# Kernel optimization log

Hardware: AMD Instinct MI355X
Metric: run time of the kernel (lower is better)

The kernel has to match this reference:

```python
import jax, jax.numpy as jnp
import numpy as np

N = 50000       # nodes
E = 400000      # edges (avg degree 8)
IN, HID, OUT, ED = 128, 256, 128, 64
EXP = 2          # GENConv MLP expansion
EPS_MSG = 1e-7   # GENConv eps added to relu(msg)
EPS_BN = 1e-5    # BatchNorm eps
EPS_SM = 1e-16   # PyG softmax denominator eps


def _lin(key, fi, fo):
    w = jax.random.normal(key, (fi, fo), jnp.float32) / np.float32(np.sqrt(fi))
    return w, jnp.zeros((fo,), jnp.float32)


def _layer_params(key, fi, fo, ed):
    ks = jax.random.split(key, 5)
    Wsrc, bsrc = _lin(ks[0], fi, fo)
    Wdst, bdst = _lin(ks[1], fi, fo)
    We, be = _lin(ks[2], ed, fo)
    W1, b1 = _lin(ks[3], fo, fo * EXP)
    W2, b2 = _lin(ks[4], fo * EXP, fo)
    g = jnp.ones((fo * EXP,), jnp.float32)   # BN gamma
    bt = jnp.zeros((fo * EXP,), jnp.float32) # BN beta
    return dict(Wsrc=Wsrc, bsrc=bsrc, Wdst=Wdst, bdst=bdst, We=We, be=be,
                W1=W1, b1=b1, g=g, bt=bt, W2=W2, b2=b2)


def setup_inputs() -> dict:
    key = jax.random.key(0)
    k0, k1, k2, k3, k4 = jax.random.split(key, 5)
    inp = {
        'x': jax.random.normal(k0, (N, IN), jnp.float32),
        'edge_index': jax.random.randint(k1, (2, E), 0, N, jnp.int32),
        'edge_attr': jax.random.normal(k2, (E, ED), jnp.float32),
    }
    for pref, p in (('l1_', _layer_params(k3, IN, HID, ED)),
                    ('l2_', _layer_params(k4, HID, OUT, ED))):
        for n, v in p.items():
            inp[pref + n] = v
    return inp


def _genconv(x, src, dst, ea, Wsrc, bsrc, Wdst, bdst, We, be, W1, b1, g, bt, W2, b2):
    n = x.shape[0]
    h = x @ Wsrc + bsrc                          # [N, F] lin_src
    e = ea @ We + be                             # [E, F] lin_edge
    msg = jax.nn.relu(h[src] + e) + EPS_MSG      # [E, F] message
    # softmax aggregation over destination nodes (t = 1.0)
    mx = jax.ops.segment_max(msg, dst, num_segments=n)
    ex = jnp.exp(msg - mx[dst])
    den = jax.ops.segment_sum(ex, dst, num_segments=n)
    alpha = ex / (den[dst] + EPS_SM)
    agg = jax.ops.segment_sum(alpha * msg, dst, num_segments=n)  # [N, F]
    out = agg + (x @ Wdst + bdst)                # residual lin_dst
    # MLP: Linear -> BatchNorm(train stats) -> ReLU -> Linear
    h1 = out @ W1 + b1                           # [N, 2F]
    mu = h1.mean(0)
    var = h1.var(0)
    h1 = (h1 - mu) * jax.lax.rsqrt(var + EPS_BN) * g + bt
    return jax.nn.relu(h1) @ W2 + b2


def reference(x, edge_index, edge_attr,
              l1_Wsrc, l1_bsrc, l1_Wdst, l1_bdst, l1_We, l1_be,
              l1_W1, l1_b1, l1_g, l1_bt, l1_W2, l1_b2,
              l2_Wsrc, l2_bsrc, l2_Wdst, l2_bdst, l2_We, l2_be,
              l2_W1, l2_b1, l2_g, l2_bt, l2_W2, l2_b2):
    src, dst = edge_index[0], edge_index[1]
    h = _genconv(x, src, dst, edge_attr,
                 l1_Wsrc, l1_bsrc, l1_Wdst, l1_bdst, l1_We, l1_be,
                 l1_W1, l1_b1, l1_g, l1_bt, l1_W2, l1_b2)
    h = jax.nn.relu(h)
    return _genconv(h, src, dst, edge_attr,
                    l2_Wsrc, l2_bsrc, l2_Wdst, l2_bdst, l2_We, l2_be,
                    l2_W1, l2_b1, l2_g, l2_bt, l2_W2, l2_b2)
```

## Files before the change

kernel.cpp:

```cpp
#include <hip/hip_runtime.h>

typedef unsigned short u16;
typedef unsigned int u32;
typedef __attribute__((ext_vector_type(8))) short sv8;
typedef __attribute__((ext_vector_type(4))) float fv4;
typedef __attribute__((ext_vector_type(4))) unsigned short us4;
typedef __attribute__((ext_vector_type(2))) unsigned short us2;

__device__ __forceinline__ u16 f2b(float x) {
    union { float f; u32 u; } a; a.f = x;
    u32 r = a.u + 0x7FFFu + ((a.u >> 16) & 1u);
    return (u16)(r >> 16);
}
__device__ __forceinline__ float b2f(u16 h) {
    union { u32 u; float f; } a; a.u = ((u32)h) << 16;
    return a.f;
}

__device__ __forceinline__ void gll16(const void* g, void* l) {
    __builtin_amdgcn_global_load_lds((__attribute__((address_space(1))) void*)g,
                                     (__attribute__((address_space(3))) void*)l,
                                     16, 0, 0);
}

template<bool AF32, bool AAFF, int EPI, bool STATS>
__global__ __launch_bounds__(256) void k_gemm(
    const void* __restrict__ Aptr, const u16* __restrict__ Wt,
    const float* __restrict__ bias, void* __restrict__ Cptr,
    int M, int K, int F,
    const float* __restrict__ sc, const float* __restrict__ sh,
    float* __restrict__ sums, float* __restrict__ sumsq)
{
    __shared__ u16 As[64][36];
    __shared__ u16 Bs[64][36];
    __shared__ u16 Cs[64][68];
    const int t = threadIdx.x, w = t >> 6, l = t & 63;
    const int n0 = blockIdx.x * 64, m0 = blockIdx.y * 64;
    const int arow = t >> 2, acol = (t & 3) << 3;
    const size_t gr = (size_t)(m0 + arow < M ? m0 + arow : M - 1);

    fv4 acc[4] = {};

    for (int k0 = 0; k0 < K; k0 += 32) {
        sv8 av;
        if constexpr (AF32) {
            const float* Af = (const float*)Aptr;
            fv4 u0 = *(const fv4*)(Af + gr * K + k0 + acol);
            fv4 u1 = *(const fv4*)(Af + gr * K + k0 + acol + 4);
            #pragma unroll
            for (int j = 0; j < 4; ++j) { av[j] = (short)f2b(u0[j]); av[j + 4] = (short)f2b(u1[j]); }
        } else if constexpr (AAFF) {
            sv8 v = *(const sv8*)((const u16*)Aptr + gr * K + k0 + acol);
            fv4 c0 = *(const fv4*)(sc + k0 + acol), c1 = *(const fv4*)(sc + k0 + acol + 4);
            fv4 d0 = *(const fv4*)(sh + k0 + acol), d1 = *(const fv4*)(sh + k0 + acol + 4);
            #pragma unroll
            for (int j = 0; j < 4; ++j) {
                av[j]     = (short)f2b(fmaxf(b2f((u16)v[j])     * c0[j] + d0[j], 0.f));
                av[j + 4] = (short)f2b(fmaxf(b2f((u16)v[j + 4]) * c1[j] + d1[j], 0.f));
            }
        } else {
            av = *(const sv8*)((const u16*)Aptr + gr * K + k0 + acol);
        }
        *(sv8*)&As[arow][acol] = av;
        *(sv8*)&Bs[arow][acol] = *(const sv8*)(Wt + (size_t)(n0 + arow) * K + k0 + acol);
        __syncthreads();

        sv8 a = *(const sv8*)&As[(w << 4) + (l & 15)][(l >> 4) << 3];
        #pragma unroll
        for (int ct = 0; ct < 4; ++ct) {
            sv8 b = *(const sv8*)&Bs[(ct << 4) + (l & 15)][(l >> 4) << 3];
            acc[ct] = __builtin_amdgcn_mfma_f32_16x16x32_bf16(a, b, acc[ct], 0, 0, 0);
        }
        __syncthreads();
    }

    const int lr0 = (w << 4) + ((l >> 4) << 2);
    #pragma unroll
    for (int ct = 0; ct < 4; ++ct) {
        const int col = (ct << 4) + (l & 15);
        const float bv = bias[n0 + col];
        float s = 0.f, s2 = 0.f;
        #pragma unroll
        for (int r = 0; r < 4; ++r) {
            const int lrow = lr0 + r;
            const bool valid = (m0 + lrow) < M;
            float v = acc[ct][r] + bv;
            if constexpr (STATS) { if (valid) { s += v; s2 += v * v; } }
            if constexpr (EPI == 1) v = fmaxf(v, 0.f);
            if constexpr (EPI == 3) {
                if (valid) ((float*)Cptr)[(size_t)(m0 + lrow) * F + n0 + col] = v;
            } else {
                Cs[lrow][col] = f2b(v);
            }
        }
        if constexpr (STATS) {
            s  += __shfl_xor(s, 16);  s  += __shfl_xor(s, 32);
            s2 += __shfl_xor(s2, 16); s2 += __shfl_xor(s2, 32);
            if (l < 16) { unsafeAtomicAdd(&sums[n0 + col], s); unsafeAtomicAdd(&sumsq[n0 + col], s2); }
        }
    }
    if constexpr (EPI != 3) {
        __syncthreads();
        const int lrow = t >> 2, c0 = (t & 3) << 4;
        if (m0 + lrow < M) {
            u16* Cb = (u16*)Cptr + (size_t)(m0 + lrow) * F + n0 + c0;
            *(sv8*)Cb       = *(const sv8*)&Cs[lrow][c0];
            *(sv8*)(Cb + 8) = *(const sv8*)&Cs[lrow][c0 + 8];
        }
    }
}

template<int FN>
__global__ __launch_bounds__(256) void k_egemm3(
    const float* __restrict__ ea, const int* __restrict__ perm,
    const u16* __restrict__ Wt, const float* __restrict__ bias,
    u16* __restrict__ Cbuf)
{
    __shared__ u16 Bs[FN * 64];
    const int t = threadIdx.x, w = t >> 6, l = t & 63;
    const int m0 = blockIdx.x * 64;

    constexpr int BISS = FN / 32;
    #pragma unroll
    for (int i = 0; i < BISS; ++i) {
        int slot = ((w * BISS + i) << 6) + l;
        int row = slot >> 3, g = (slot & 7) ^ (row & 7);
        gll16(Wt + (size_t)row * 64 + g * 8, Bs + ((w * BISS + i) << 6) * 8);
    }

    const int g0 = l >> 4;
    const int gr = m0 + (w << 4) + (l & 15);
    const int prow = perm[gr];
    const float* ar = ea + (size_t)prow * 64 + (g0 << 3);
    fv4 u0 = *(const fv4*)ar;
    fv4 u1 = *(const fv4*)(ar + 4);
    fv4 u2 = *(const fv4*)(ar + 32);
    fv4 u3 = *(const fv4*)(ar + 36);
    sv8 a0, a1;
    #pragma unroll
    for (int j = 0; j < 4; ++j) {
        a0[j] = (short)f2b(u0[j]); a0[j + 4] = (short)f2b(u1[j]);
        a1[j] = (short)f2b(u2[j]); a1[j + 4] = (short)f2b(u3[j]);
    }
    __syncthreads();

    fv4 acc[FN / 16];
    #pragma unroll
    for (int ct = 0; ct < FN / 16; ++ct) {
        int Brow = (ct << 4) + (l & 15);
        sv8 b0 = *(const sv8*)&Bs[(Brow * 8 + ((g0)     ^ (Brow & 7))) * 8];
        sv8 b1 = *(const sv8*)&Bs[(Brow * 8 + ((g0 + 4) ^ (Brow & 7))) * 8];
        fv4 z = {};
        z = __builtin_amdgcn_mfma_f32_16x16x32_bf16(a0, b0, z, 0, 0, 0);
        acc[ct] = __builtin_amdgcn_mfma_f32_16x16x32_bf16(a1, b1, z, 0, 0, 0);
    }

    const int r0 = (w << 4) + ((l >> 4) << 2);
    #pragma unroll
    for (int ct = 0; ct < FN / 16; ++ct) {
        const int col = (ct << 4) + (l & 15);
        const float bv = bias[col];
        #pragma unroll
        for (int r = 0; r < 4; ++r) {
            const int row = m0 + r0 + r;
            u32 my = (u32)f2b(acc[ct][r] + bv);
            u32 ot = (u32)__shfl_xor((int)my, 1);
            if (!(l & 1))
                *(u32*)(Cbuf + (size_t)row * FN + col) = (my & 0xFFFFu) | (ot << 16);
        }
    }
}

__global__ void k_hist(const int* __restrict__ dst, int* __restrict__ counts, int E) {
    int i = blockIdx.x * 256 + threadIdx.x;
    if (i < E) atomicAdd(&counts[dst[i]], 1);
}

__global__ __launch_bounds__(256) void k_psum(const int* __restrict__ counts,
                                              int* __restrict__ bsum, int n) {
    int i = blockIdx.x * 256 + threadIdx.x;
    int v = (i < n) ? counts[i] : 0;
    #pragma unroll
    for (int o = 1; o < 64; o <<= 1) v += __shfl_xor(v, o);
    __shared__ int ws[4];
    if ((threadIdx.x & 63) == 0) ws[threadIdx.x >> 6] = v;
    __syncthreads();
    if (threadIdx.x == 0) bsum[blockIdx.x] = ws[0] + ws[1] + ws[2] + ws[3];
}

__global__ __launch_bounds__(256) void k_bscan(const int* __restrict__ bsum,
                                               int* __restrict__ boff, int nb) {
    __shared__ int sm[256];
    int t = threadIdx.x;
    int v = (t < nb) ? bsum[t] : 0;
    sm[t] = v; __syncthreads();
    #pragma unroll
    for (int o = 1; o < 256; o <<= 1) {
        int u = (t >= o) ? sm[t - o] : 0;
        __syncthreads();
        sm[t] += u;
        __syncthreads();
    }
    if (t < nb) boff[t] = sm[t] - v;
}

__global__ __launch_bounds__(256) void k_windp(const int* __restrict__ counts,
                                               const int* __restrict__ boff,
                                               int* __restrict__ indptr,
                                               int* __restrict__ cursors, int n) {
    __shared__ int sm[256];
    const int t = threadIdx.x, i = blockIdx.x * 256 + t;
    int v = (i < n) ? counts[i] : 0;
    sm[t] = v; __syncthreads();
    #pragma unroll
    for (int o = 1; o < 256; o <<= 1) {
        int u = (t >= o) ? sm[t - o] : 0;
        __syncthreads();
        sm[t] += u;
        __syncthreads();
    }
    int excl = sm[t] - v + boff[blockIdx.x];
    if (i < n) { indptr[i] = excl; cursors[i] = excl; }
    if (i == n - 1) indptr[n] = excl + v;
}

__global__ void k_scatter(const int* __restrict__ dst, const int* __restrict__ src,
                          int* __restrict__ cursors, int* __restrict__ perm,
                          int* __restrict__ srcp, int E) {
    int i = blockIdx.x * 256 + threadIdx.x;
    if (i < E) {
        int p = atomicAdd(&cursors[dst[i]], 1);
        perm[p] = i;
        srcp[p] = src[i];
    }
}

template<int F, int VPT>
__global__ __launch_bounds__(256) void k_agg(
    const u16* __restrict__ e, const u16* __restrict__ hhd,
    const int* __restrict__ srcp, const int* __restrict__ indptr,
    u16* __restrict__ out, int N)
{
    const int nid = blockIdx.x * 4 + (threadIdx.x >> 6);
    if (nid >= N) return;
    const int c0 = (threadIdx.x & 63) * VPT;
    const int S = 2 * F;
    const int p0 = indptr[nid], p1 = indptr[nid + 1];
    float den[VPT] = {}, num[VPT] = {};
    for (int p = p0; p < p1; ++p) {
        const int s = srcp[p];
        u16 ev[VPT], hv[VPT];
        if constexpr (VPT == 4) {
            *(us4*)ev = *(const us4*)&e[(size_t)p * F + c0];
            *(us4*)hv = *(const us4*)&hhd[(size_t)s * S + c0];
        } else {
            *(us2*)ev = *(const us2*)&e[(size_t)p * F + c0];
            *(us2*)hv = *(const us2*)&hhd[(size_t)s * S + c0];
        }
        #pragma unroll
        for (int j = 0; j < VPT; ++j) {
            float x = fmaxf(b2f(ev[j]) + b2f(hv[j]), 0.f) + 1e-7f;
            float ex = __expf(x);
            den[j] += ex;
            num[j] += ex * x;
        }
    }
    #pragma unroll
    for (int j = 0; j < VPT; ++j) {
        float o = num[j] / (den[j] + 1e-16f) + b2f(hhd[(size_t)nid * S + F + c0 + j]);
        out[(size_t)nid * F + c0 + j] = f2b(o);
    }
}

struct WtDesc { const float* W; u16* D; int K; int F; int end; };
struct WtPack { WtDesc d[10]; };

__global__ void k_wtall(WtPack p, int total) {
    int i = blockIdx.x * 256 + threadIdx.x;
    if (i >= total) return;
    int s = 0, base = 0;
    while (i >= p.d[s].end) { base = p.d[s].end; ++s; }
    int loc = i - base;
    int K = p.d[s].K, F = p.d[s].F;
    int f = loc / K, k = loc - f * K;
    p.d[s].D[loc] = f2b(p.d[s].W[(size_t)k * F + f]);
}

__global__ void k_bcat(const float* __restrict__ bsrc1, const float* __restrict__ bdst1,
                       const float* __restrict__ bsrc2, const float* __restrict__ bdst2,
                       float* __restrict__ bcat1, float* __restrict__ bcat2) {
    int t = threadIdx.x;
    bcat1[t] = bsrc1[t];
    bcat1[256 + t] = bdst1[t];
    if (t < 128) {
        bcat2[t] = bsrc2[t];
        bcat2[128 + t] = bdst2[t];
    }
}

__global__ void k_bnfinal(const float* __restrict__ sums, const float* __restrict__ sumsq,
                          const float* __restrict__ g, const float* __restrict__ bt,
                          float* __restrict__ scale, float* __restrict__ shift,
                          int C, float invN)
{
    int c = blockIdx.x * 256 + threadIdx.x;
    if (c < C) {
        float mu  = sums[c] * invN;
        float var = sumsq[c] * invN - mu * mu;
        float s   = g[c] * rsqrtf(var + 1e-5f);
        scale[c] = s;
        shift[c] = bt[c] - mu * s;
    }
}

extern "C" void kernel_launch(void* const* d_in, const int* in_sizes, int n_in,
                              void* d_out, int out_size, void* d_ws, size_t ws_size,
                              hipStream_t stream)
{
    const int IN = 128, HID = 256, OUT = 128, ED = 64;
    const int N = in_sizes[0] / IN;
    const int E = in_sizes[1] / 2;

    const float* x   = (const float*)d_in[0];
    const int*   src = (const int*)d_in[1];
    const int*   dst = src + E;
    const float* ea  = (const float*)d_in[2];
    auto F32 = [&](int i) { return (const float*)d_in[i]; };
    const float *Wsrc1 = F32(3),  *bsrc1 = F32(4),  *Wdst1 = F32(5),  *bdst1 = F32(6),
                *We1   = F32(7),  *be1   = F32(8),  *W11   = F32(9),  *b11   = F32(10),
                *g1    = F32(11), *bt1   = F32(12), *W21   = F32(13), *b21   = F32(14);
    const float *Wsrc2 = F32(15), *bsrc2 = F32(16), *Wdst2 = F32(17), *bdst2 = F32(18),
                *We2   = F32(19), *be2   = F32(20), *W12   = F32(21), *b12   = F32(22),
                *g2    = F32(23), *bt2   = F32(24), *W22   = F32(25), *b22   = F32(26);

    char* wp = (char*)d_ws;
    auto carve = [&](size_t bytes) -> void* {
        void* r = (void*)wp; wp += (bytes + 255) & ~(size_t)255; return r;
    };
    u16* wcat1  = (u16*)carve((size_t)HID * IN * 2);
    u16* wdst1t = (u16*)carve((size_t)HID * IN * 2);
    u16* we1t   = (u16*)carve((size_t)HID * ED * 2);
    u16* w11t   = (u16*)carve((size_t)(2 * HID) * HID * 2);
    u16* w21t   = (u16*)carve((size_t)HID * (2 * HID) * 2);
    u16* wcat2  = (u16*)carve((size_t)OUT * HID * 2);
    u16* wdst2t = (u16*)carve((size_t)OUT * HID * 2);
    u16* we2t   = (u16*)carve((size_t)OUT * ED * 2);
    u16* w12t   = (u16*)carve((size_t)(2 * OUT) * OUT * 2);
    u16* w22t   = (u16*)carve((size_t)OUT * (2 * OUT) * 2);
    int* counts  = (int*)carve((size_t)N * 4);
    int* indptr  = (int*)carve((size_t)(N + 1) * 4);
    int* cursors = (int*)carve((size_t)N * 4);
    int* perm    = (int*)carve((size_t)E * 4);
    int* srcp    = (int*)carve((size_t)E * 4);
    int* bsum    = (int*)carve((size_t)256 * 4);
    int* boff    = (int*)carve((size_t)256 * 4);
    u16* hhd  = (u16*)carve((size_t)N * 512 * 2);
    u16* x2   = (u16*)carve((size_t)N * HID * 2);
    u16* ebuf = (u16*)carve((size_t)E * HID * 2);
    float* stats1 = (float*)carve((size_t)1024 * 4);
    float* stats2 = (float*)carve((size_t)512 * 4);
    float* ss1    = (float*)carve((size_t)1024 * 4);
    float* ss2    = (float*)carve((size_t)512 * 4);
    float* bcat1  = (float*)carve((size_t)512 * 4);
    float* bcat2  = (float*)carve((size_t)256 * 4);
    u16* h1 = ebuf;

    hipMemsetAsync(counts, 0, (size_t)N * 4, stream);
    hipMemsetAsync(stats1, 0, (size_t)(1024 + 512) * 4, stream);
    k_hist<<<dim3((E + 255) / 256), dim3(256), 0, stream>>>(dst, counts, E);
    const int nb = (N + 255) / 256;
    k_psum<<<dim3(nb), dim3(256), 0, stream>>>(counts, bsum, N);
    k_bscan<<<dim3(1), dim3(256), 0, stream>>>(bsum, boff, nb);
    k_windp<<<dim3(nb), dim3(256), 0, stream>>>(counts, boff, indptr, cursors, N);
    k_scatter<<<dim3((E + 255) / 256), dim3(256), 0, stream>>>(dst, src, cursors, perm, srcp, E);

    WtPack wpk; int acc_end = 0;
    auto addw = [&](int idx, const float* W, u16* D, int K, int F) {
        acc_end += K * F;
        wpk.d[idx] = WtDesc{W, D, K, F, acc_end};
    };
    addw(0, Wsrc1, wcat1,  IN, HID);   addw(1, Wdst1, wdst1t, IN, HID);
    addw(2, We1,   we1t,   ED, HID);   addw(3, W11,   w11t,   HID, 2 * HID);
    addw(4, W21,   w21t,   2 * HID, HID);
    addw(5, Wsrc2, wcat2,  HID, OUT);  addw(6, Wdst2, wdst2t, HID, OUT);
    addw(7, We2,   we2t,   ED, OUT);   addw(8, W12,   w12t,   OUT, 2 * OUT);
    addw(9, W22,   w22t,   2 * OUT, OUT);
    k_wtall<<<dim3((acc_end + 255) / 256), dim3(256), 0, stream>>>(wpk, acc_end);
    k_bcat<<<dim3(1), dim3(256), 0, stream>>>(bsrc1, bdst1, bsrc2, bdst2, bcat1, bcat2);

    const int gm = (N + 63) / 64;

    k_gemm<true, false, 0, false><<<dim3(8, gm), dim3(256), 0, stream>>>(
        x, wcat1, bcat1, hhd, N, IN, 512, nullptr, nullptr, nullptr, nullptr);
    k_egemm3<256><<<dim3(E / 64), dim3(256), 0, stream>>>(ea, perm, we1t, be1, ebuf);
    k_agg<256, 4><<<dim3((N + 3) / 4), dim3(256), 0, stream>>>(ebuf, hhd, srcp, indptr, x2, N);
    k_gemm<false, false, 0, true><<<dim3(8, gm), dim3(256), 0, stream>>>(
        x2, w11t, b11, h1, N, HID, 512, nullptr, nullptr, stats1, stats1 + 512);
    k_bnfinal<<<dim3(2), dim3(256), 0, stream>>>(
        stats1, stats1 + 512, g1, bt1, ss1, ss1 + 512, 512, 1.f / N);
    k_gemm<false, true, 1, false><<<dim3(4, gm), dim3(256), 0, stream>>>(
        h1, w21t, b21, x2, N, 512, HID, ss1, ss1 + 512, nullptr, nullptr);

    k_gemm<false, false, 0, false><<<dim3(4, gm), dim3(256), 0, stream>>>(
        x2, wcat2, bcat2, hhd, N, HID, 256, nullptr, nullptr, nullptr, nullptr);
    k_egemm3<128><<<dim3(E / 64), dim3(256), 0, stream>>>(ea, perm, we2t, be2, ebuf);
    k_agg<128, 2><<<dim3((N + 3) / 4), dim3(256), 0, stream>>>(ebuf, hhd, srcp, indptr, x2, N);
    k_gemm<false, false, 0, true><<<dim3(4, gm), dim3(256), 0, stream>>>(
        x2, w12t, b12, h1, N, OUT, 256, nullptr, nullptr, stats2, stats2 + 256);
    k_bnfinal<<<dim3(1), dim3(256), 0, stream>>>(
        stats2, stats2 + 256, g2, bt2, ss2, ss2 + 256, 256, 1.f / N);
    k_gemm<false, true, 3, false><<<dim3(2, gm), dim3(256), 0, stream>>>(
        h1, w22t, b22, d_out, N, HID, OUT, ss2, ss2 + 256, nullptr, nullptr);
}
```

Before: 699.9 us.

## Keep full weight panel resident in LDS with persistent row-tile GEMM loop

Replaces the K-tiled GEMM, which staged A and B through LDS with two barriers per k-step, by a kernel that loads a 64-column weight panel for the whole K into swizzled LDS once via global_load_lds. Each block then loops over many row tiles, streaming A straight from global memory into registers. MFMA operands are swapped so each lane holds four consecutive output columns, which allows vector stores without the LDS staging buffer. BatchNorm statistics are accumulated per block and reduced with fewer atomics. The cost is large LDS usage for K=512 (64 KB), which lowers occupancy, and a fixed grid size that may underfill or imbalance the GPU.

Result: slower. 833.7 us (+19.1%).

```diff
diff --git a/kernel.cpp b/kernel.cpp
--- a/kernel.cpp
+++ b/kernel.cpp
@@ -23,89 +23,112 @@
                                      16, 0, 0);
 }
 
-template<bool AF32, bool AAFF, int EPI, bool STATS>
-__global__ __launch_bounds__(256) void k_gemm(
+template<int K, int EPI, bool AF32, bool AAFF, bool STATS>
+__global__ __launch_bounds__(256) void k_ngemm(
     const void* __restrict__ Aptr, const u16* __restrict__ Wt,
     const float* __restrict__ bias, void* __restrict__ Cptr,
-    int M, int K, int F,
+    int M, int F,
     const float* __restrict__ sc, const float* __restrict__ sh,
     float* __restrict__ sums, float* __restrict__ sumsq)
 {
-    __shared__ u16 As[64][36];
-    __shared__ u16 Bs[64][36];
-    __shared__ u16 Cs[64][68];
+    constexpr int GPR = K / 8;
+    __shared__ u16 Ws[64 * K];
     const int t = threadIdx.x, w = t >> 6, l = t & 63;
-    const int n0 = blockIdx.x * 64, m0 = blockIdx.y * 64;
-    const int arow = t >> 2, acol = (t & 3) << 3;
-    const size_t gr = (size_t)(m0 + arow < M ? m0 + arow : M - 1);
-
-    fv4 acc[4] = {};
-
-    for (int k0 = 0; k0 < K; k0 += 32) {
-        sv8 av;
-        if constexpr (AF32) {
-            const float* Af = (const float*)Aptr;
-            fv4 u0 = *(const fv4*)(Af + gr * K + k0 + acol);
-            fv4 u1 = *(const fv4*)(Af + gr * K + k0 + acol + 4);
+    const int q = l >> 4;
+    const int n0 = blockIdx.x * 64;
+
+    #pragma unroll
+    for (int i = 0; i < K / 32; ++i) {
+        int slotbase = (w * (K / 32) + i) << 6;
+        int slot = slotbase + l;
+        int row = slot / GPR;
+        int g = slot & (GPR - 1);
+        int gs = (g & ~7) | ((g & 7) ^ (row & 7));
+        gll16(Wt + (size_t)(n0 + row) * K + gs * 8, Ws + slotbase * 8);
+    }
+    __syncthreads();
+
+    float sacc[16] = {}, s2acc[16] = {};
+    const int lrow = (w << 4) + (l & 15);
+
+    for (int m0 = blockIdx.y * 64; m0 < M; m0 += gridDim.y * 64) {
+        const int row = m0 + lrow;
+        const bool valid = row < M;
+        const size_t gr = valid ? (size_t)row : (size_t)(M - 1);
+        fv4 acc[4] = {};
+
+        #pragma unroll
+        for (int kk = 0; kk < K / 32; ++kk) {
+            const int kb = kk * 32 + q * 8;
+            sv8 a;
+            if constexpr (AF32) {
+                const float* Af = (const float*)Aptr;
+                fv4 u0 = *(const fv4*)(Af + gr * K + kb);
+                fv4 u1 = *(const fv4*)(Af + gr * K + kb + 4);
+                #pragma unroll
+                for (int j = 0; j < 4; ++j) { a[j] = (short)f2b(u0[j]); a[j + 4] = (short)f2b(u1[j]); }
+            } else if constexpr (AAFF) {
+                sv8 v = *(const sv8*)((const u16*)Aptr + gr * K + kb);
+                fv4 c0 = *(const fv4*)(sc + kb), c1 = *(const fv4*)(sc + kb + 4);
+                fv4 d0 = *(const fv4*)(sh + kb), d1 = *(const fv4*)(sh + kb + 4);
+                #pragma unroll
+                for (int j = 0; j < 4; ++j) {
+                    a[j]     = (short)f2b(fmaxf(b2f((u16)v[j])     * c0[j] + d0[j], 0.f));
+                    a[j + 4] = (short)f2b(fmaxf(b2f((u16)v[j + 4]) * c1[j] + d1[j], 0.f));
+                }
+            } else {
+                a = *(const sv8*)((const u16*)Aptr + gr * K + kb);
+            }
             #pragma unroll
-            for (int j = 0; j < 4; ++j) { av[j] = (short)f2b(u0[j]); av[j + 4] = (short)f2b(u1[j]); }
-        } else if constexpr (AAFF) {
-            sv8 v = *(const sv8*)((const u16*)Aptr + gr * K + k0 + acol);
-            fv4 c0 = *(const fv4*)(sc + k0 + acol), c1 = *(const fv4*)(sc + k0 + acol + 4);
-            fv4 d0 = *(const fv4*)(sh + k0 + acol), d1 = *(const fv4*)(sh + k0 + acol + 4);
-            #pragma unroll
-            for (int j = 0; j < 4; ++j) {
-                av[j]     = (short)f2b(fmaxf(b2f((u16)v[j])     * c0[j] + d0[j], 0.f));
-                av[j + 4] = (short)f2b(fmaxf(b2f((u16)v[j + 4]) * c1[j] + d1[j], 0.f));
+            for (int ct = 0; ct < 4; ++ct) {
+                const int col = (ct << 4) + (l & 15);
+                const int g = kk * 4 + q;
+                const int gs = (g & ~7) | ((g & 7) ^ (col & 7));
+                sv8 b = *(const sv8*)&Ws[col * K + gs * 8];
+                acc[ct] = __builtin_amdgcn_mfma_f32_16x16x32_bf16(b, a, acc[ct], 0, 0, 0);
             }
-        } else {
-            av = *(const sv8*)((const u16*)Aptr + gr * K + k0 + acol);
         }
-        *(sv8*)&As[arow][acol] = av;
-        *(sv8*)&Bs[arow][acol] = *(const sv8*)(Wt + (size_t)(n0 + arow) * K + k0 + acol);
-        __syncthreads();
-
-        sv8 a = *(const sv8*)&As[(w << 4) + (l & 15)][(l >> 4) << 3];
+
         #pragma unroll
         for (int ct = 0; ct < 4; ++ct) {
-            sv8 b = *(const sv8*)&Bs[(ct << 4) + (l & 15)][(l >> 4) << 3];
-            acc[ct] = __builtin_amdgcn_mfma_f32_16x16x32_bf16(a, b, acc[ct], 0, 0, 0);
-        }
-        __syncthreads();
-    }
-
-    const int lr0 = (w << 4) + ((l >> 4) << 2);
-    #pragma unroll
-    for (int ct = 0; ct < 4; ++ct) {
-        const int col = (ct << 4) + (l & 15);
-        const float bv = bias[n0 + col];
-        float s = 0.f, s2 = 0.f;
-        #pragma unroll
-        for (int r = 0; r < 4; ++r) {
-            const int lrow = lr0 + r;
-            const bool valid = (m0 + lrow) < M;
-            float v = acc[ct][r] + bv;
-            if constexpr (STATS) { if (valid) { s += v; s2 += v * v; } }
-            if constexpr (EPI == 1) v = fmaxf(v, 0.f);
-            if constexpr (EPI == 3) {
-                if (valid) ((float*)Cptr)[(size_t)(m0 + lrow) * F + n0 + col] = v;
-            } else {
-                Cs[lrow][col] = f2b(v);
+            const int colb = n0 + (ct << 4) + (q << 2);
+            fv4 bv = *(const fv4*)(bias + colb);
+            float v[4];
+            #pragma unroll
+            for (int r = 0; r < 4; ++r) {
+                v[r] = acc[ct][r] + bv[r];
+                if constexpr (STATS) {
+                    if (valid) { sacc[ct * 4 + r] += v[r]; s2acc[ct * 4 + r] += v[r] * v[r]; }
+                }
+                if constexpr (EPI == 1) v[r] = fmaxf(v[r], 0.f);
+            }
+            if (valid) {
+                if constexpr (EPI == 3) {
+                    fv4 o = { v[0], v[1], v[2], v[3] };
+                    *(fv4*)((float*)Cptr + (size_t)row * F + colb) = o;
+                } else {
+                    u16 o[4];
+                    #pragma unroll
+                    for (int r = 0; r < 4; ++r) o[r] = f2b(v[r]);
+                    *(us4*)((u16*)Cptr + (size_t)row * F + colb) = *(us4*)o;
+                }
             }
         }
-        if constexpr (STATS) {
-            s  += __shfl_xor(s, 16);  s  += __shfl_xor(s, 32);
-            s2 += __shfl_xor(s2, 16); s2 += __shfl_xor(s2, 32);
-            if (l < 16) { unsafeAtomicAdd(&sums[n0 + col], s); unsafeAtomicAdd(&sumsq[n0 + col], s2); }
-        }
-    }
-    if constexpr (EPI != 3) {
-        __syncthreads();
-        const int lrow = t >> 2, c0 = (t & 3) << 4;
-        if (m0 + lrow < M) {
-            u16* Cb = (u16*)Cptr + (size_t)(m0 + lrow) * F + n0 + c0;
-            *(sv8*)Cb       = *(const sv8*)&Cs[lrow][c0];
-            *(sv8*)(Cb + 8) = *(const sv8*)&Cs[lrow][c0 + 8];
+    }
+
+    if constexpr (STATS) {
+        #pragma unroll
+        for (int i = 0; i < 16; ++i) {
+            float s = sacc[i], s2 = s2acc[i];
+            s  += __shfl_xor(s, 1);  s  += __shfl_xor(s, 2);
+            s  += __shfl_xor(s, 4);  s  += __shfl_xor(s, 8);
+            s2 += __shfl_xor(s2, 1); s2 += __shfl_xor(s2, 2);
+            s2 += __shfl_xor(s2, 4); s2 += __shfl_xor(s2, 8);
+            if ((l & 15) == 0) {
+                const int col = n0 + ((i >> 2) << 4) + (q << 2) + (i & 3);
+                unsafeAtomicAdd(&sums[col], s);
+                unsafeAtomicAdd(&sumsq[col], s2);
+            }
         }
     }
 }
@@ -118,6 +141,7 @@
 {
     __shared__ u16 Bs[FN * 64];
     const int t = threadIdx.x, w = t >> 6, l = t & 63;
+    const int q = l >> 4;
     const int m0 = blockIdx.x * 64;
 
     constexpr int BISS = FN / 32;
@@ -128,10 +152,9 @@
         gll16(Wt + (size_t)row * 64 + g * 8, Bs + ((w * BISS + i) << 6) * 8);
     }
 
-    const int g0 = l >> 4;
     const int gr = m0 + (w << 4) + (l & 15);
     const int prow = perm[gr];
-    const float* ar = ea + (size_t)prow * 64 + (g0 << 3);
+    const float* ar = ea + (size_t)prow * 64 + (q << 3);
     fv4 u0 = *(const fv4*)ar;
     fv4 u1 = *(const fv4*)(ar + 4);
     fv4 u2 = *(const fv4*)(ar + 32);
@@ -148,26 +171,21 @@
     #pragma unroll
     for (int ct = 0; ct < FN / 16; ++ct) {
         int Brow = (ct << 4) + (l & 15);
-        sv8 b0 = *(const sv8*)&Bs[(Brow * 8 + ((g0)     ^ (Brow & 7))) * 8];
-        sv8 b1 = *(const sv8*)&Bs[(Brow * 8 + ((g0 + 4) ^ (Brow & 7))) * 8];
+        sv8 b0 = *(const sv8*)&Bs[(Brow * 8 + ((q)     ^ (Brow & 7))) * 8];
+        sv8 b1 = *(const sv8*)&Bs[(Brow * 8 + ((q + 4) ^ (Brow & 7))) * 8];
         fv4 z = {};
-        z = __builtin_amdgcn_mfma_f32_16x16x32_bf16(a0, b0, z, 0, 0, 0);
-        acc[ct] = __builtin_amdgcn_mfma_f32_16x16x32_bf16(a1, b1, z, 0, 0, 0);
-    }
-
-    const int r0 = (w << 4) + ((l >> 4) << 2);
+        z = __builtin_amdgcn_mfma_f32_16x16x32_bf16(b0, a0, z, 0, 0, 0);
+        acc[ct] = __builtin_amdgcn_mfma_f32_16x16x32_bf16(b1, a1, z, 0, 0, 0);
+    }
+
     #pragma unroll
     for (int ct = 0; ct < FN / 16; ++ct) {
-        const int col = (ct << 4) + (l & 15);
-        const float bv = bias[col];
+        const int colb = (ct << 4) + (q << 2);
+        fv4 bv = *(const fv4*)(bias + colb);
+        u16 o[4];
         #pragma unroll
-        for (int r = 0; r < 4; ++r) {
-            const int row = m0 + r0 + r;
-            u32 my = (u32)f2b(acc[ct][r] + bv);
-            u32 ot = (u32)__shfl_xor((int)my, 1);
-            if (!(l & 1))
-                *(u32*)(Cbuf + (size_t)row * FN + col) = (my & 0xFFFFu) | (ot << 16);
-        }
+        for (int r = 0; r < 4; ++r) o[r] = f2b(acc[ct][r] + bv[r]);
+        *(us4*)(Cbuf + (size_t)gr * FN + colb) = *(us4*)o;
     }
 }
 
@@ -388,27 +406,25 @@
     k_wtall<<<dim3((acc_end + 255) / 256), dim3(256), 0, stream>>>(wpk, acc_end);
     k_bcat<<<dim3(1), dim3(256), 0, stream>>>(bsrc1, bdst1, bsrc2, bdst2, bcat1, bcat2);
 
-    const int gm = (N + 63) / 64;
-
-    k_gemm<true, false, 0, false><<<dim3(8, gm), dim3(256), 0, stream>>>(
-        x, wcat1, bcat1, hhd, N, IN, 512, nullptr, nullptr, nullptr, nullptr);
+    k_ngemm<128, 0, true, false, false><<<dim3(8, 120), dim3(256), 0, stream>>>(
+        x, wcat1, bcat1, hhd, N, 512, nullptr, nullptr, nullptr, nullptr);
     k_egemm3<256><<<dim3(E / 64), dim3(256), 0, stream>>>(ea, perm, we1t, be1, ebuf);
     k_agg<256, 4><<<dim3((N + 3) / 4), dim3(256), 0, stream>>>(ebuf, hhd, srcp, indptr, x2, N);
-    k_gemm<false, false, 0, true><<<dim3(8, gm), dim3(256), 0, stream>>>(
-        x2, w11t, b11, h1, N, HID, 512, nullptr, nullptr, stats1, stats1 + 512);
+    k_ngemm<256, 0, false, false, true><<<dim3(8, 120), dim3(256), 0, stream>>>(
+        x2, w11t, b11, h1, N, 512, nullptr, nullptr, stats1, stats1 + 512);
     k_bnfinal<<<dim3(2), dim3(256), 0, stream>>>(
         stats1, stats1 + 512, g1, bt1, ss1, ss1 + 512, 512, 1.f / N);
-    k_gemm<false, true, 1, false><<<dim3(4, gm), dim3(256), 0, stream>>>(
-        h1, w21t, b21, x2, N, 512, HID, ss1, ss1 + 512, nullptr, nullptr);
-
-    k_gemm<false, false, 0, false><<<dim3(4, gm), dim3(256), 0, stream>>>(
-        x2, wcat2, bcat2, hhd, N, HID, 256, nullptr, nullptr, nullptr, nullptr);
+    k_ngemm<512, 1, false, true, false><<<dim3(4, 240), dim3(256), 0, stream>>>(
+        h1, w21t, b21, x2, N, 256, ss1, ss1 + 512, nullptr, nullptr);
+
+    k_ngemm<256, 0, false, false, false><<<dim3(4, 240), dim3(256), 0, stream>>>(
+        x2, wcat2, bcat2, hhd, N, 256, nullptr, nullptr, nullptr, nullptr);
     k_egemm3<128><<<dim3(E / 64), dim3(256), 0, stream>>>(ea, perm, we2t, be2, ebuf);
     k_agg<128, 2><<<dim3((N + 3) / 4), dim3(256), 0, stream>>>(ebuf, hhd, srcp, indptr, x2, N);
-    k_gemm<false, false, 0, true><<<dim3(4, gm), dim3(256), 0, stream>>>(
-        x2, w12t, b12, h1, N, OUT, 256, nullptr, nullptr, stats2, stats2 + 256);
+    k_ngemm<128, 0, false, false, true><<<dim3(4, 240), dim3(256), 0, stream>>>(
+        x2, w12t, b12, h1, N, 256, nullptr, nullptr, stats2, stats2 + 256);
     k_bnfinal<<<dim3(1), dim3(256), 0, stream>>>(
         stats2, stats2 + 256, g2, bt2, ss2, ss2 + 256, 256, 1.f / N);
-    k_gemm<false, true, 3, false><<<dim3(2, gm), dim3(256), 0, stream>>>(
-        h1, w22t, b22, d_out, N, HID, OUT, ss2, ss2 + 256, nullptr, nullptr);
-}
+    k_ngemm<256, 3, false, true, false><<<dim3(2, 480), dim3(256), 0, stream>>>(
+        h1, w22t, b22, d_out, N, 128, ss2, ss2 + 256, nullptr, nullptr);
+}
```
